# Optimization experiments

Hardware: AMD Instinct MI355X
Metric: run time of the kernel (lower is better)

## Reference

```python
import jax, jax.numpy as jnp
import numpy as np

DEPTH, HEADS, DIM_HEAD = 6, 12, 64
DIM, MLP, FEAT = 768, 3072, 1000
B, N = 32, 196
EPS = 1e-5


def layernorm(x, g, b):
    m = jnp.mean(x, axis=-1, keepdims=True)
    v = jnp.var(x, axis=-1, keepdims=True)
    return (x - m) * jax.lax.rsqrt(v + EPS) * g + b


def setup_inputs() -> dict:
    key = jax.random.key(0)
    ks = jax.random.split(key, 8)
    s = 0.02
    return {
        "x": jax.random.normal(ks[0], (B, N, DIM), jnp.float32),
        "cls_token": jax.random.normal(ks[1], (1, 1, DIM), jnp.float32),
        "ln1_g": jnp.ones((DEPTH, DIM), jnp.float32),
        "ln1_b": jnp.zeros((DEPTH, DIM), jnp.float32),
        "w_qkv": jax.random.normal(ks[2], (DEPTH, DIM, 3 * HEADS * DIM_HEAD), jnp.float32) * s,
        "reattn_w": jax.random.normal(ks[3], (DEPTH, HEADS, HEADS), jnp.float32),
        "reattn_g": jnp.ones((DEPTH, HEADS), jnp.float32),
        "reattn_b": jnp.zeros((DEPTH, HEADS), jnp.float32),
        "w_out": jax.random.normal(ks[4], (DEPTH, HEADS * DIM_HEAD, DIM), jnp.float32) * s,
        "b_out": jnp.zeros((DEPTH, DIM), jnp.float32),
        "ln2_g": jnp.ones((DEPTH, DIM), jnp.float32),
        "ln2_b": jnp.zeros((DEPTH, DIM), jnp.float32),
        "w1": jax.random.normal(ks[5], (DEPTH, DIM, MLP), jnp.float32) * s,
        "b1": jnp.zeros((DEPTH, MLP), jnp.float32),
        "w2": jax.random.normal(ks[6], (DEPTH, MLP, DIM), jnp.float32) * s,
        "b2": jnp.zeros((DEPTH, DIM), jnp.float32),
        "lnf_g": jnp.ones((DIM,), jnp.float32),
        "lnf_b": jnp.zeros((DIM,), jnp.float32),
        "w_head": jax.random.normal(ks[7], (DIM, FEAT), jnp.float32) * s,
        "b_head": jnp.zeros((FEAT,), jnp.float32),
    }


def _forward(x, cls_token, ln1_g, ln1_b, w_qkv, reattn_w, reattn_g, reattn_b,
             w_out, b_out, ln2_g, ln2_b, w1, b1, w2, b2, lnf_g, lnf_b, w_head, b_head):
    b = x.shape[0]
    cls = jnp.broadcast_to(cls_token, (b, 1, DIM))
    x = jnp.concatenate([cls, x], axis=1)  # (B, N+1, DIM)
    n = x.shape[1]
    scale = DIM_HEAD ** -0.5
    for l in range(DEPTH):
        h = layernorm(x, ln1_g[l], ln1_b[l])
        qkv = h @ w_qkv[l]                       # (B, n, 3*H*Dh)
        qkv = qkv.reshape(b, n, 3, HEADS, DIM_HEAD)
        q, k, v = (qkv[:, :, i].transpose(0, 2, 1, 3) for i in range(3))  # b h n d
        dots = jnp.einsum('bhid,bhjd->bhij', q, k) * scale
        attn = jax.nn.softmax(dots, axis=-1)
        attn = jnp.einsum('bhij,hg->bgij', attn, reattn_w[l])
        # per-head LayerNorm: normalize over head axis (axis=1)
        m = jnp.mean(attn, axis=1, keepdims=True)
        var = jnp.var(attn, axis=1, keepdims=True)
        attn = (attn - m) * jax.lax.rsqrt(var + EPS)
        attn = attn * reattn_g[l][None, :, None, None] + reattn_b[l][None, :, None, None]
        out = jnp.einsum('bhij,bhjd->bhid', attn, v)
        out = out.transpose(0, 2, 1, 3).reshape(b, n, HEADS * DIM_HEAD)
        x = x + out @ w_out[l] + b_out[l]
        h = layernorm(x, ln2_g[l], ln2_b[l])
        h = jax.nn.gelu(h @ w1[l] + b1[l], approximate=False)
        x = x + h @ w2[l] + b2[l]
    pooled = x[:, 0]  # cls pool
    return layernorm(pooled, lnf_g, lnf_b) @ w_head + b_head


def reference(x, cls_token, ln1_g, ln1_b, w_qkv, reattn_w, reattn_g, reattn_b,
              w_out, b_out, ln2_g, ln2_b, w1, b1, w2, b2, lnf_g, lnf_b, w_head, b_head):
    return _forward(x, cls_token, ln1_g, ln1_b, w_qkv, reattn_w, reattn_g, reattn_b,
                    w_out, b_out, ln2_g, ln2_b, w1, b1, w2, b2, lnf_g, lnf_b, w_head, b_head)
```

## Files before the change

kernel.cpp:

```cpp
#include <hip/hip_runtime.h>
#include <cstdint>

typedef __bf16 bf16_t;
typedef __bf16 bf16x8 __attribute__((ext_vector_type(8)));
typedef float  f32x4  __attribute__((ext_vector_type(4)));
typedef unsigned int u32;

#define DEPTH 6
#define HEADS 12
#define DH    64
#define DIM   768
#define MLPD  3072
#define FEAT  1000
#define BATCH 32
#define SEQ   197
#define NP    224
#define TOK   (BATCH*SEQ)

__device__ __forceinline__ f32x4 zero4() {
    f32x4 z; z[0] = 0.f; z[1] = 0.f; z[2] = 0.f; z[3] = 0.f; return z;
}

__device__ __forceinline__ f32x4 mfma16(bf16x8 a, bf16x8 b, f32x4 c) {
    return __builtin_amdgcn_mfma_f32_16x16x32_bf16(a, b, c, 0, 0, 0);
}

typedef const __attribute__((address_space(1))) u32* gas_ptr;
typedef __attribute__((address_space(3))) u32*       las_ptr;
__device__ __forceinline__ void gload16(const bf16_t* g, bf16_t* l) {
    __builtin_amdgcn_global_load_lds((gas_ptr)g, (las_ptr)l, 16, 0, 0);
}

__global__ __launch_bounds__(256) void concat_k(const float* __restrict__ x,
                                                const float* __restrict__ cls,
                                                float* __restrict__ xbuf) {
    int idx = blockIdx.x * 256 + threadIdx.x;
    int col = idx % DIM;
    int row = idx / DIM;
    int b = row / SEQ, p = row % SEQ;
    xbuf[idx] = (p == 0) ? cls[col] : x[(b * 196 + p - 1) * DIM + col];
}

__global__ __launch_bounds__(256) void tcvt_k(const float* __restrict__ W,
                                              bf16_t* __restrict__ Wt,
                                              int K, int N) {
    __shared__ float t[32][33];
    int n0 = blockIdx.x * 32, k0 = blockIdx.y * 32;
    int c = threadIdx.x & 31, r = threadIdx.x >> 5;
#pragma unroll
    for (int i = 0; i < 4; i++) {
        int k = k0 + r + i * 8, n = n0 + c;
        t[r + i * 8][c] = (n < N) ? W[k * N + n] : 0.f;
    }
    __syncthreads();
#pragma unroll
    for (int i = 0; i < 4; i++) {
        int n = n0 + r + i * 8, k = k0 + c;
        if (n < N) Wt[n * K + k] = (bf16_t)t[c][r + i * 8];
    }
}

__global__ __launch_bounds__(256) void tcvtall_k(const float* __restrict__ wq,
                                                 const float* __restrict__ wo,
                                                 const float* __restrict__ w1p,
                                                 const float* __restrict__ w2p,
                                                 bf16_t* __restrict__ wt) {
    int id = blockIdx.x;
    const float* W; int K, N, ntx, rid; long doff;
    if (id < 1728)      { W = wq;  K = 768;  N = 2304; doff = 0;       ntx = 72; rid = id; }
    else if (id < 2304) { W = wo;  K = 768;  N = 768;  doff = 1769472; ntx = 24; rid = id - 1728; }
    else if (id < 4608) { W = w1p; K = 768;  N = 3072; doff = 2359296; ntx = 96; rid = id - 2304; }
    else                { W = w2p; K = 3072; N = 768;  doff = 4718592; ntx = 24; rid = id - 4608; }
    int n0 = (rid % ntx) * 32, k0 = (rid / ntx) * 32;
    __shared__ float t[32][33];
    int c = threadIdx.x & 31, r = threadIdx.x >> 5;
#pragma unroll
    for (int i = 0; i < 4; i++)
        t[r + i * 8][c] = W[(long)(k0 + r + i * 8) * N + n0 + c];
    __syncthreads();
#pragma unroll
    for (int i = 0; i < 4; i++)
        wt[doff + (long)(n0 + r + i * 8) * K + k0 + c] = (bf16_t)t[c][r + i * 8];
}

__global__ __launch_bounds__(256) void ln_k(const float* __restrict__ x, long row_stride,
                                            const float* __restrict__ g,
                                            const float* __restrict__ b,
                                            bf16_t* __restrict__ out) {
    int row = blockIdx.x;
    const float* xr = x + (long)row * row_stride;
    int t = threadIdx.x;
    float v0 = xr[t], v1 = xr[t + 256], v2 = xr[t + 512];
    float s  = v0 + v1 + v2;
    float sq = v0 * v0 + v1 * v1 + v2 * v2;
#pragma unroll
    for (int o = 1; o < 64; o <<= 1) { s += __shfl_xor(s, o); sq += __shfl_xor(sq, o); }
    __shared__ float ss[4], sqs[4];
    int w = t >> 6;
    if ((t & 63) == 0) { ss[w] = s; sqs[w] = sq; }
    __syncthreads();
    s  = ss[0] + ss[1] + ss[2] + ss[3];
    sq = sqs[0] + sqs[1] + sqs[2] + sqs[3];
    float m  = s * (1.f / 768.f);
    float rs = rsqrtf(sq * (1.f / 768.f) - m * m + 1e-5f);
    bf16_t* orow = out + (long)row * DIM;
    orow[t]       = (bf16_t)((v0 - m) * rs * g[t]       + b[t]);
    orow[t + 256] = (bf16_t)((v1 - m) * rs * g[t + 256] + b[t + 256]);
    orow[t + 512] = (bf16_t)((v2 - m) * rs * g[t + 512] + b[t + 512]);
}

template <int MODE>
__global__ __launch_bounds__(512) void gemm_k(const bf16_t* __restrict__ A,
                                              const bf16_t* __restrict__ Bt,
                                              const float* __restrict__ bias,
                                              float* __restrict__ Cf,
                                              bf16_t* __restrict__ Cb,
                                              int M, int N, int Kstride, int Klen) {
    __shared__ bf16_t sA[2][128][32];
    __shared__ bf16_t sB[2][256][32];
    int tid = threadIdx.x;
    int bm = blockIdx.x * 128, bn = blockIdx.y * 256;
    long koff = (long)blockIdx.z * Klen;
    int wave = tid >> 6, lane = tid & 63;
    int wm = (wave >> 2) * 64, wn = (wave & 3) * 64;
    int la = lane & 15, lb = lane >> 4;

    int trow = tid >> 2, colE = (tid & 3) * 8;
    int rowA = bm + trow; if (rowA > M - 1) rowA = M - 1;
    int rowB0 = bn + trow, rowB1 = bn + 128 + trow;

    f32x4 acc[4][4];
#pragma unroll
    for (int m = 0; m < 4; m++)
#pragma unroll
        for (int n = 0; n < 4; n++) acc[m][n] = zero4();

    auto stage = [&](int buf, long k0) {
        gload16(A  + (long)rowA  * Kstride + k0 + colE, &sA[buf][0][0] + wave * 512);
        gload16(Bt + (long)rowB0 * Kstride + k0 + colE, &sB[buf][0][0] + wave * 512);
        gload16(Bt + (long)rowB1 * Kstride + k0 + colE, &sB[buf][0][0] + 4096 + wave * 512);
    };

    int nt = Klen >> 5;
    stage(0, koff);
    __syncthreads();
    for (int t = 0; t < nt; t++) {
        int cur = t & 1;
        if (t + 1 < nt) stage(cur ^ 1, koff + ((long)(t + 1) << 5));
        bf16x8 af[4], bfr[4];
#pragma unroll
        for (int m = 0; m < 4; m++) af[m]  = *(const bf16x8*)&sA[cur][wm + m * 16 + la][lb * 8];
#pragma unroll
        for (int n = 0; n < 4; n++) bfr[n] = *(const bf16x8*)&sB[cur][wn + n * 16 + la][lb * 8];
#pragma unroll
        for (int m = 0; m < 4; m++)
#pragma unroll
            for (int n = 0; n < 4; n++)
                acc[m][n] = mfma16(af[m], bfr[n], acc[m][n]);
        __syncthreads();
    }

    long kout = (long)blockIdx.z * M * (long)N;
#pragma unroll
    for (int m = 0; m < 4; m++) {
#pragma unroll
        for (int n = 0; n < 4; n++) {
            int ib = bm + wm + m * 16 + lb * 4;
            int jb = bn + wn + n * 16 + la;
            float bv = (MODE == 1 || MODE == 2) ? bias[jb] : 0.f;
#pragma unroll
            for (int r = 0; r < 4; r++) {
                int i = ib + r;
                if (i >= M) continue;
                float v = acc[m][n][r];
                if (MODE == 0) {
                    Cb[(long)i * N + jb] = (bf16_t)v;
                } else if (MODE == 1) {
                    Cf[(long)i * N + jb] += v + bv;
                } else if (MODE == 2) {
                    float u = v + bv;
                    Cb[(long)i * N + jb] = (bf16_t)(0.5f * u * (1.f + erff(u * 0.70710678118f)));
                } else {
                    Cf[kout + (long)i * N + jb] = v;
                }
            }
        }
    }
}

template <int NC, bool DOLN>
__global__ __launch_bounds__(256) void redln_k(float* __restrict__ xbuf,
                                               const float* __restrict__ part,
                                               const float* __restrict__ bias,
                                               const float* __restrict__ g,
                                               const float* __restrict__ b,
                                               bf16_t* __restrict__ out) {
    int row = blockIdx.x, t = threadIdx.x;
    long base = (long)row * DIM;
    const long total = (long)TOK * DIM;
    float v[3];
    float s = 0.f, sq = 0.f;
#pragma unroll
    for (int q = 0; q < 3; q++) {
        int col = t + q * 256;
        long idx = base + col;
        float val = xbuf[idx] + bias[col];
#pragma unroll
        for (int k = 0; k < NC; k++) val += part[idx + (long)k * total];
        xbuf[idx] = val;
        v[q] = val; s += val; sq += val * val;
    }
    if (DOLN) {
#pragma unroll
        for (int o = 1; o < 64; o <<= 1) { s += __shfl_xor(s, o); sq += __shfl_xor(sq, o); }
        __shared__ float ss[4], sqs[4];
        int w = t >> 6;
        if ((t & 63) == 0) { ss[w] = s; sqs[w] = sq; }
        __syncthreads();
        s  = ss[0] + ss[1] + ss[2] + ss[3];
        sq = sqs[0] + sqs[1] + sqs[2] + sqs[3];
        float m  = s * (1.f / 768.f);
        float rs = rsqrtf(sq * (1.f / 768.f) - m * m + 1e-5f);
        bf16_t* orow = out + base;
#pragma unroll
        for (int q = 0; q < 3; q++) {
            int col = t + q * 256;
            orow[col] = (bf16_t)((v[q] - m) * rs * g[col] + b[col]);
        }
    }
}

__global__ __launch_bounds__(256) void gemm_h(const bf16_t* __restrict__ A,
                                              const bf16_t* __restrict__ Bt,
                                              const float* __restrict__ bias,
                                              float* __restrict__ Cf,
                                              int M, int N, int K) {
    __shared__ bf16_t sA[2][128][32];
    __shared__ bf16_t sB[2][128][32];
    int tid = threadIdx.x;
    int bm = blockIdx.x * 128, bn = blockIdx.y * 128;
    int wave = tid >> 6, lane = tid & 63;
    int wm = (wave >> 1) * 64, wn = (wave & 1) * 64;
    int la = lane & 15, lb = lane >> 4;
    int rowA[2], rowB[2], colE[2];
#pragma unroll
    for (int q = 0; q < 2; q++) {
        int li = (wave * 2 + q) * 64 + lane;
        int row = li >> 2;
        colE[q] = (li & 3) * 8;
        int ar = bm + row; if (ar > M - 1) ar = M - 1;
        int br = bn + row; if (br > N - 1) br = N - 1;
        rowA[q] = ar; rowB[q] = br;
    }
    f32x4 acc[4][4];
#pragma unroll
    for (int m = 0; m < 4; m++)
#pragma unroll
        for (int n = 0; n < 4; n++) acc[m][n] = zero4();
    int nt = K >> 5;
#pragma unroll
    for (int q = 0; q < 2; q++) {
        gload16(A  + (long)rowA[q] * K + colE[q], &sA[0][0][0] + (wave * 2 + q) * 512);
        gload16(Bt + (long)rowB[q] * K + colE[q], &sB[0][0][0] + (wave * 2 + q) * 512);
    }
    __syncthreads();
    for (int t = 0; t < nt; t++) {
        int cur = t & 1;
        if (t + 1 < nt) {
            int k0 = (t + 1) << 5;
#pragma unroll
            for (int q = 0; q < 2; q++) {
                gload16(A  + (long)rowA[q] * K + k0 + colE[q], &sA[cur ^ 1][0][0] + (wave * 2 + q) * 512);
                gload16(Bt + (long)rowB[q] * K + k0 + colE[q], &sB[cur ^ 1][0][0] + (wave * 2 + q) * 512);
            }
        }
        bf16x8 af[4], bfr[4];
#pragma unroll
        for (int m = 0; m < 4; m++) af[m]  = *(const bf16x8*)&sA[cur][wm + m * 16 + la][lb * 8];
#pragma unroll
        for (int n = 0; n < 4; n++) bfr[n] = *(const bf16x8*)&sB[cur][wn + n * 16 + la][lb * 8];
#pragma unroll
        for (int m = 0; m < 4; m++)
#pragma unroll
            for (int n = 0; n < 4; n++)
                acc[m][n] = mfma16(af[m], bfr[n], acc[m][n]);
        __syncthreads();
    }
#pragma unroll
    for (int m = 0; m < 4; m++) {
#pragma unroll
        for (int n = 0; n < 4; n++) {
            int ib = bm + wm + m * 16 + lb * 4;
            int jb = bn + wn + n * 16 + la;
            if (jb >= N) continue;
            float bv = bias[jb];
#pragma unroll
            for (int r = 0; r < 4; r++) {
                int i = ib + r;
                if (i >= M) continue;
                Cf[(long)i * N + jb] = acc[m][n][r] + bv;
            }
        }
    }
}

__global__ __launch_bounds__(256) void qk_k(const bf16_t* __restrict__ qkv,
                                            bf16_t* __restrict__ dots) {
    int bh = blockIdx.z;
    int b = bh / HEADS, h = bh % HEADS;
    int i0 = blockIdx.x * 64, j0 = blockIdx.y * 64;
    __shared__ bf16_t sQ[64][32], sK[64][32];
    int tid = threadIdx.x, wave = tid >> 6, lane = tid & 63;
    int wm = (wave >> 1) * 32, wn = (wave & 1) * 32;
    int la = lane & 15, lb = lane >> 4;
    f32x4 acc[2][2];
#pragma unroll
    for (int m = 0; m < 2; m++)
#pragma unroll
        for (int n = 0; n < 2; n++) acc[m][n] = zero4();

    int row = tid >> 2, col = (tid & 3) * 8;
    int qi = i0 + row; if (qi > SEQ - 1) qi = SEQ - 1;
    int kj = j0 + row; if (kj > SEQ - 1) kj = SEQ - 1;
    const bf16_t* qsrc = qkv + (((b * SEQ + qi) * 3 + 0) * HEADS + h) * DH + col;
    const bf16_t* ksrc = qkv + (((b * SEQ + kj) * 3 + 1) * HEADS + h) * DH + col;

#pragma unroll
    for (int d0 = 0; d0 < 64; d0 += 32) {
        *(bf16x8*)&sQ[row][col] = *(const bf16x8*)(qsrc + d0);
        *(bf16x8*)&sK[row][col] = *(const bf16x8*)(ksrc + d0);
        __syncthreads();
        bf16x8 af[2], bfr[2];
#pragma unroll
        for (int m = 0; m < 2; m++) af[m]  = *(const bf16x8*)&sQ[wm + m * 16 + la][lb * 8];
#pragma unroll
        for (int n = 0; n < 2; n++) bfr[n] = *(const bf16x8*)&sK[wn + n * 16 + la][lb * 8];
#pragma unroll
        for (int m = 0; m < 2; m++)
#pragma unroll
            for (int n = 0; n < 2; n++)
                acc[m][n] = mfma16(af[m], bfr[n], acc[m][n]);
        __syncthreads();
    }
#pragma unroll
    for (int m = 0; m < 2; m++)
#pragma unroll
        for (int n = 0; n < 2; n++)
#pragma unroll
            for (int r = 0; r < 4; r++) {
                int i = i0 + wm + m * 16 + lb * 4 + r;
                int j = j0 + wn + n * 16 + la;
                if (i < SEQ && j < SEQ)
                    dots[((long)bh * SEQ + i) * NP + j] = (bf16_t)(acc[m][n][r] * 0.125f);
            }
}

__global__ __launch_bounds__(256) void smre_k(const bf16_t* __restrict__ dots,
                                              const float* __restrict__ W,
                                              const float* __restrict__ gg,
                                              const float* __restrict__ bb,
                                              bf16_t* __restrict__ attn2) {
    __shared__ float sm[HEADS][NP];
    __shared__ float sW[HEADS * HEADS];
    __shared__ float sg[HEADS], sb[HEADS];
    int tid = threadIdx.x;
    if (tid < HEADS * HEADS) sW[tid] = W[tid];
    if (tid < HEADS) { sg[tid] = gg[tid]; sb[tid] = bb[tid]; }
    int bi = blockIdx.x;
    int b = bi / SEQ, i = bi % SEQ;
    int wave = tid >> 6, lane = tid & 63;

    for (int h = wave; h < HEADS; h += 4) {
        const bf16_t* p = dots + ((long)(b * HEADS + h) * SEQ + i) * NP;
        float v[4], e[4];
#pragma unroll
        for (int q = 0; q < 4; q++) { int j = lane + 64 * q; v[q] = (j < SEQ) ? (float)p[j] : -3.0e38f; }
        float mx = fmaxf(fmaxf(v[0], v[1]), fmaxf(v[2], v[3]));
#pragma unroll
        for (int o = 1; o < 64; o <<= 1) mx = fmaxf(mx, __shfl_xor(mx, o));
        float s = 0.f;
#pragma unroll
        for (int q = 0; q < 4; q++) {
            int j = lane + 64 * q;
            e[q] = (j < SEQ) ? __expf(v[q] - mx) : 0.f;
            s += e[q];
        }
#pragma unroll
        for (int o = 1; o < 64; o <<= 1) s += __shfl_xor(s, o);
        float inv = 1.f / s;
#pragma unroll
        for (int q = 0; q < 4; q++) { int j = lane + 64 * q; if (j < NP) sm[h][j] = e[q] * inv; }
    }
    __syncthreads();

    int j = tid;
    if (j >= NP) return;
    bool valid = j < SEQ;
    float vals[HEADS];
#pragma unroll
    for (int h = 0; h < HEADS; h++) vals[h] = valid ? sm[h][j] : 0.f;
    float mix[HEADS];
    float s = 0.f, sq = 0.f;
#pragma unroll
    for (int g = 0; g < HEADS; g++) {
        float a = 0.f;
#pragma unroll
        for (int h = 0; h < HEADS; h++) a += vals[h] * sW[h * HEADS + g];
        mix[g] = a; s += a; sq += a * a;
    }
    float m  = s * (1.f / 12.f);
    float rs = rsqrtf(sq * (1.f / 12.f) - m * m + 1e-5f);
    long base = ((long)(b * HEADS) * SEQ + i) * NP + j;
    const long hs = (long)SEQ * NP;
#pragma unroll
    for (int g = 0; g < HEADS; g++) {
        float o = valid ? ((mix[g] - m) * rs * sg[g] + sb[g]) : 0.f;
        attn2[base + g * hs] = (bf16_t)o;
    }
}

__global__ __launch_bounds__(256) void pv_k(const bf16_t* __restrict__ attn2,
                                            const bf16_t* __restrict__ qkv,
                                            bf16_t* __restrict__ aout) {
    int bh = blockIdx.y;
    int b = bh / HEADS, h = bh % HEADS;
    int i0 = blockIdx.x * 64;
    __shared__ bf16_t sP[64][32];
    __shared__ bf16_t sVt[64][32];
    int tid = threadIdx.x, wave = tid >> 6, lane = tid & 63;
    int wm = (wave >> 1) * 32, wn = (wave & 1) * 32;
    int la = lane & 15, lb = lane >> 4;
    f32x4 acc[2][2];
#pragma unroll
    for (int m = 0; m < 2; m++)
#pragma unroll
        for (int n = 0; n < 2; n++) acc[m][n] = zero4();

    int prow = tid >> 2, pcol = (tid & 3) * 8;
    int pi = i0 + prow; if (pi > SEQ - 1) pi = SEQ - 1;
    const bf16_t* psrc = attn2 + ((long)bh * SEQ + pi) * NP + pcol;
    int jl = tid >> 3, dblk = (tid & 7) * 8;
    int jlx = jl ^ ((tid & 3) << 3);

    for (int j0 = 0; j0 < NP; j0 += 32) {
        *(bf16x8*)&sP[prow][pcol] = *(const bf16x8*)(psrc + j0);
        int jg = j0 + jl;
        bf16x8 vv;
#pragma unroll
        for (int e = 0; e < 8; e++) vv[e] = (bf16_t)0.f;
        if (jg < SEQ)
            vv = *(const bf16x8*)(qkv + (((b * SEQ + jg) * 3 + 2) * HEADS + h) * DH + dblk);
#pragma unroll
        for (int e = 0; e < 8; e++) sVt[dblk + e][jlx] = vv[e];
        __syncthreads();
        bf16x8 af[2], bfr[2];
#pragma unroll
        for (int m = 0; m < 2; m++) af[m] = *(const bf16x8*)&sP[wm + m * 16 + la][lb * 8];
#pragma unroll
        for (int n = 0; n < 2; n++) {
            int rowd = wn + n * 16 + la;
            int colj = (lb * 8) ^ (((rowd >> 3) & 3) << 3);
            bfr[n] = *(const bf16x8*)&sVt[rowd][colj];
        }
#pragma unroll
        for (int m = 0; m < 2; m++)
#pragma unroll
            for (int n = 0; n < 2; n++)
                acc[m][n] = mfma16(af[m], bfr[n], acc[m][n]);
        __syncthreads();
    }
#pragma unroll
    for (int m = 0; m < 2; m++)
#pragma unroll
        for (int n = 0; n < 2; n++)
#pragma unroll
            for (int r = 0; r < 4; r++) {
                int i = i0 + wm + m * 16 + lb * 4 + r;
                int d = wn + n * 16 + la;
                if (i < SEQ)
                    aout[((long)b * SEQ + i) * DIM + h * DH + d] = (bf16_t)acc[m][n][r];
            }
}

extern "C" void kernel_launch(void* const* d_in, const int* in_sizes, int n_in,
                              void* d_out, int out_size, void* d_ws, size_t ws_size,
                              hipStream_t stream) {
    const float* x        = (const float*)d_in[0];
    const float* cls      = (const float*)d_in[1];
    const float* ln1_g    = (const float*)d_in[2];
    const float* ln1_b    = (const float*)d_in[3];
    const float* w_qkv    = (const float*)d_in[4];
    const float* reattn_w = (const float*)d_in[5];
    const float* reattn_g = (const float*)d_in[6];
    const float* reattn_b = (const float*)d_in[7];
    const float* w_out    = (const float*)d_in[8];
    const float* b_out    = (const float*)d_in[9];
    const float* ln2_g    = (const float*)d_in[10];
    const float* ln2_b    = (const float*)d_in[11];
    const float* w1       = (const float*)d_in[12];
    const float* b1       = (const float*)d_in[13];
    const float* w2       = (const float*)d_in[14];
    const float* b2       = (const float*)d_in[15];
    const float* lnf_g    = (const float*)d_in[16];
    const float* lnf_b    = (const float*)d_in[17];
    const float* w_head   = (const float*)d_in[18];
    const float* b_head   = (const float*)d_in[19];
    float* out = (float*)d_out;

    char* p = (char*)d_ws;
    auto alloc = [&](size_t bytes) -> char* {
        char* r = p;
        p += (bytes + 255) & ~(size_t)255;
        return r;
    };
    bf16_t* wt      = (bf16_t*)alloc(2ULL * 7077888);
    bf16_t* wt_head = (bf16_t*)alloc(2ULL * FEAT * DIM);
    float*  xbuf    = (float*)alloc(4ULL * TOK * DIM);
    bf16_t* h_ln    = (bf16_t*)alloc(2ULL * TOK * DIM);
    bf16_t* qkv     = (bf16_t*)alloc(2ULL * TOK * 3 * DIM);
    char*   dreg    = alloc(2ULL * TOK * MLPD);
    bf16_t* dots    = (bf16_t*)dreg;
    bf16_t* h_mid   = (bf16_t*)dreg;
    float*  part_op = (float*)dreg;
    bf16_t* attn2   = (bf16_t*)alloc(2ULL * BATCH * HEADS * SEQ * NP);
    bf16_t* aout    = (bf16_t*)alloc(2ULL * TOK * DIM);
    alloc(4ULL * 4 * TOK * DIM - 2ULL * BATCH * HEADS * SEQ * NP - 2ULL * TOK * DIM);
    float*  part_m2 = (float*)attn2;

    dim3 B256(256), B512(512);
    concat_k<<<(TOK * DIM) / 256, B256, 0, stream>>>(x, cls, xbuf);
    tcvt_k<<<dim3((FEAT + 31) / 32, DIM / 32), B256, 0, stream>>>(w_head, wt_head, DIM, FEAT);

    bf16_t* wqkv_t = wt;
    bf16_t* wout_t = wt + 1769472;
    bf16_t* w1_t   = wt + 2359296;
    bf16_t* w2_t   = wt + 4718592;

    ln_k<<<TOK, B256, 0, stream>>>(xbuf, DIM, ln1_g, ln1_b, h_ln);

    for (int l = 0; l < DEPTH; l++) {
        tcvtall_k<<<6912, B256, 0, stream>>>(w_qkv + (long)l * DIM * 2304,
                                             w_out + (long)l * DIM * DIM,
                                             w1 + (long)l * DIM * MLPD,
                                             w2 + (long)l * MLPD * DIM, wt);
        gemm_k<0><<<dim3(50, 9), B512, 0, stream>>>(h_ln, wqkv_t, nullptr, nullptr, qkv, TOK, 2304, DIM, DIM);
        qk_k<<<dim3(4, 4, BATCH * HEADS), B256, 0, stream>>>(qkv, dots);
        smre_k<<<TOK, B256, 0, stream>>>(
            dots, reattn_w + l * HEADS * HEADS, reattn_g + l * HEADS, reattn_b + l * HEADS, attn2);
        pv_k<<<dim3(4, BATCH * HEADS), B256, 0, stream>>>(attn2, qkv, aout);
        gemm_k<3><<<dim3(50, 3, 2), B512, 0, stream>>>(aout, wout_t, nullptr, part_op, nullptr,
                                                       TOK, DIM, DIM, DIM / 2);
        redln_k<2, true><<<TOK, B256, 0, stream>>>(xbuf, part_op, b_out + l * DIM,
                                                   ln2_g + l * DIM, ln2_b + l * DIM, h_ln);
        gemm_k<2><<<dim3(50, 12), B512, 0, stream>>>(h_ln, w1_t, b1 + l * MLPD, nullptr, h_mid, TOK, MLPD, DIM, DIM);
        gemm_k<3><<<dim3(50, 3, 4), B512, 0, stream>>>(h_mid, w2_t, nullptr, part_m2, nullptr,
                                                       TOK, DIM, MLPD, MLPD / 4);
        if (l < DEPTH - 1)
            redln_k<4, true><<<TOK, B256, 0, stream>>>(xbuf, part_m2, b2 + l * DIM,
                                                       ln1_g + (l + 1) * DIM, ln1_b + (l + 1) * DIM, h_ln);
        else
            redln_k<4, false><<<TOK, B256, 0, stream>>>(xbuf, part_m2, b2 + l * DIM,
                                                        nullptr, nullptr, nullptr);
    }

    ln_k<<<BATCH, B256, 0, stream>>>(xbuf, (long)SEQ * DIM, lnf_g, lnf_b, h_ln);
    gemm_h<<<dim3(1, 8), B256, 0, stream>>>(h_ln, wt_head, b_head, out, BATCH, FEAT, DIM);
}
```

Baseline: 1.751 ms.

## Restructure GEMM into per-wave private LDS tiles without block barriers

The GEMM kernel now gives each of four waves its own private shared-memory region and has each wave stage only the A and B rows it consumes. This lets the block-wide __syncthreads be replaced by per-wave s_waitcnt vmcnt counters. Shared-memory columns are XOR-swizzled to cut bank conflicts, and the block tile shrinks to 128x128 with 256 threads, so the launch grids double in N. The cost is that each wave reloads data its neighbours also use, losing the A/B sharing across waves and raising global and L2 traffic. Correctness relies on the async LDS loads finishing in order and on the hand-written vmcnt counts being right.

```diff
diff --git a/kernel.cpp b/kernel.cpp
--- a/kernel.cpp
+++ b/kernel.cpp
@@ -110,24 +110,25 @@
 }
 
 template <int MODE>
-__global__ __launch_bounds__(512) void gemm_k(const bf16_t* __restrict__ A,
-                                              const bf16_t* __restrict__ Bt,
-                                              const float* __restrict__ bias,
-                                              float* __restrict__ Cf,
-                                              bf16_t* __restrict__ Cb,
-                                              int M, int N, int Kstride, int Klen) {
-    __shared__ bf16_t sA[2][128][32];
-    __shared__ bf16_t sB[2][256][32];
+__global__ __launch_bounds__(256) void gemmP_k(const bf16_t* __restrict__ A,
+                                               const bf16_t* __restrict__ Bt,
+                                               const float* __restrict__ bias,
+                                               float* __restrict__ Cf,
+                                               bf16_t* __restrict__ Cb,
+                                               int M, int N, int Kstride, int Klen) {
+    __shared__ bf16_t smem[4 * 8192];
     int tid = threadIdx.x;
-    int bm = blockIdx.x * 128, bn = blockIdx.y * 256;
+    int bm = blockIdx.x * 128, bn = blockIdx.y * 128;
     long koff = (long)blockIdx.z * Klen;
     int wave = tid >> 6, lane = tid & 63;
-    int wm = (wave >> 2) * 64, wn = (wave & 3) * 64;
+    int wm = (wave >> 1) * 64, wn = (wave & 1) * 64;
     int la = lane & 15, lb = lane >> 4;
-
-    int trow = tid >> 2, colE = (tid & 3) * 8;
-    int rowA = bm + trow; if (rowA > M - 1) rowA = M - 1;
-    int rowB0 = bn + trow, rowB1 = bn + 128 + trow;
+    bf16_t* ws = smem + wave * 8192;
+
+    int srow = lane >> 2;
+    int scol = ((lane & 3) ^ ((lane >> 3) & 3)) * 8;
+    int rA0 = bm + wm + srow;
+    int rB0 = bn + wn + srow;
 
     f32x4 acc[4][4];
 #pragma unroll
@@ -135,29 +136,43 @@
 #pragma unroll
         for (int n = 0; n < 4; n++) acc[m][n] = zero4();
 
-    auto stage = [&](int buf, long k0) {
-        gload16(A  + (long)rowA  * Kstride + k0 + colE, &sA[buf][0][0] + wave * 512);
-        gload16(Bt + (long)rowB0 * Kstride + k0 + colE, &sB[buf][0][0] + wave * 512);
-        gload16(Bt + (long)rowB1 * Kstride + k0 + colE, &sB[buf][0][0] + 4096 + wave * 512);
+    const int NT = Klen >> 5;
+
+    auto stage = [&](int buf, int kt) {
+        long k0 = koff + ((long)kt << 5);
+        bf16_t* dA = ws + buf * 4096;
+        bf16_t* dB = dA + 2048;
+#pragma unroll
+        for (int i = 0; i < 4; i++) {
+            int ra = rA0 + i * 16; if (ra > M - 1) ra = M - 1;
+            gload16(A  + (long)ra * Kstride + k0 + scol, dA + i * 512);
+            gload16(Bt + (long)(rB0 + i * 16) * Kstride + k0 + scol, dB + i * 512);
+        }
     };
 
-    int nt = Klen >> 5;
-    stage(0, koff);
-    __syncthreads();
-    for (int t = 0; t < nt; t++) {
+    int rslot = (lb ^ ((la >> 1) & 3)) << 3;
+
+    stage(0, 0);
+    for (int t = 0; t < NT; t++) {
         int cur = t & 1;
-        if (t + 1 < nt) stage(cur ^ 1, koff + ((long)(t + 1) << 5));
+        if (t + 1 < NT) {
+            stage(cur ^ 1, t + 1);
+            asm volatile("s_waitcnt vmcnt(8)" ::: "memory");
+        } else {
+            asm volatile("s_waitcnt vmcnt(0)" ::: "memory");
+        }
+        const bf16_t* cA = ws + cur * 4096;
+        const bf16_t* cB = cA + 2048;
         bf16x8 af[4], bfr[4];
 #pragma unroll
-        for (int m = 0; m < 4; m++) af[m]  = *(const bf16x8*)&sA[cur][wm + m * 16 + la][lb * 8];
-#pragma unroll
-        for (int n = 0; n < 4; n++) bfr[n] = *(const bf16x8*)&sB[cur][wn + n * 16 + la][lb * 8];
+        for (int m = 0; m < 4; m++) af[m]  = *(const bf16x8*)(cA + (m * 16 + la) * 32 + rslot);
+#pragma unroll
+        for (int n = 0; n < 4; n++) bfr[n] = *(const bf16x8*)(cB + (n * 16 + la) * 32 + rslot);
 #pragma unroll
         for (int m = 0; m < 4; m++)
 #pragma unroll
             for (int n = 0; n < 4; n++)
                 acc[m][n] = mfma16(af[m], bfr[n], acc[m][n]);
-        __syncthreads();
     }
 
     long kout = (long)blockIdx.z * M * (long)N;
@@ -527,7 +542,7 @@
     alloc(4ULL * 4 * TOK * DIM - 2ULL * BATCH * HEADS * SEQ * NP - 2ULL * TOK * DIM);
     float*  part_m2 = (float*)attn2;
 
-    dim3 B256(256), B512(512);
+    dim3 B256(256);
     concat_k<<<(TOK * DIM) / 256, B256, 0, stream>>>(x, cls, xbuf);
     tcvt_k<<<dim3((FEAT + 31) / 32, DIM / 32), B256, 0, stream>>>(w_head, wt_head, DIM, FEAT);
 
@@ -543,18 +558,18 @@
                                              w_out + (long)l * DIM * DIM,
                                              w1 + (long)l * DIM * MLPD,
                                              w2 + (long)l * MLPD * DIM, wt);
-        gemm_k<0><<<dim3(50, 9), B512, 0, stream>>>(h_ln, wqkv_t, nullptr, nullptr, qkv, TOK, 2304, DIM, DIM);
+        gemmP_k<0><<<dim3(50, 18), B256, 0, stream>>>(h_ln, wqkv_t, nullptr, nullptr, qkv, TOK, 2304, DIM, DIM);
         qk_k<<<dim3(4, 4, BATCH * HEADS), B256, 0, stream>>>(qkv, dots);
         smre_k<<<TOK, B256, 0, stream>>>(
             dots, reattn_w + l * HEADS * HEADS, reattn_g + l * HEADS, reattn_b + l * HEADS, attn2);
         pv_k<<<dim3(4, BATCH * HEADS), B256, 0, stream>>>(attn2, qkv, aout);
-        gemm_k<3><<<dim3(50, 3, 2), B512, 0, stream>>>(aout, wout_t, nullptr, part_op, nullptr,
-                                                       TOK, DIM, DIM, DIM / 2);
+        gemmP_k<3><<<dim3(50, 6, 2), B256, 0, stream>>>(aout, wout_t, nullptr, part_op, nullptr,
+                                                        TOK, DIM, DIM, DIM / 2);
         redln_k<2, true><<<TOK, B256, 0, stream>>>(xbuf, part_op, b_out + l * DIM,
                                                    ln2_g + l * DIM, ln2_b + l * DIM, h_ln);
-        gemm_k<2><<<dim3(50, 12), B512, 0, stream>>>(h_ln, w1_t, b1 + l * MLPD, nullptr, h_mid, TOK, MLPD, DIM, DIM);
-        gemm_k<3><<<dim3(50, 3, 4), B512, 0, stream>>>(h_mid, w2_t, nullptr, part_m2, nullptr,
-                                                       TOK, DIM, MLPD, MLPD / 4);
+        gemmP_k<2><<<dim3(50, 24), B256, 0, stream>>>(h_ln, w1_t, b1 + l * MLPD, nullptr, h_mid, TOK, MLPD, DIM, DIM);
+        gemmP_k<3><<<dim3(50, 6, 4), B256, 0, stream>>>(h_mid, w2_t, nullptr, part_m2, nullptr,
+                                                        TOK, DIM, MLPD, MLPD / 4);
         if (l < DEPTH - 1)
             redln_k<4, true><<<TOK, B256, 0, stream>>>(xbuf, part_m2, b2 + l * DIM,
                                                        ln1_g + (l + 1) * DIM, ln1_b + (l + 1) * DIM, h_ln);
```

Measured after the change: 2.164 ms. 23.6% more time.
